# Performance work log

Measured on AMD Instinct MI355X. Metric: run time of the kernel, lower is better.

## Reference

```python
import jax, jax.numpy as jnp
import numpy as np

S, B, H2 = 2048, 16, 1024   # seq_len, batch, 2*hidden_dim
H = H2 // 2                  # hidden_dim
N = 4096                     # number of spans with nonempty tags
T = 8192                     # total number of target tags (ragged, flattened)
L = 256                      # label_dim
V = 50000                    # vocab size
GAMMA = 1.0


def setup_inputs() -> dict:
    key = jax.random.key(0)
    ks = jax.random.split(key, 10)
    hidden = jax.random.normal(ks[0], (S, B, H2), jnp.float32)
    W1 = jax.random.normal(ks[1], (L, H2), jnp.float32) * (1.0 / np.sqrt(H2))
    b1 = jnp.zeros((L,), jnp.float32)
    W2 = jax.random.normal(ks[2], (V, L), jnp.float32) * (1.0 / np.sqrt(L))
    b2 = jnp.zeros((V,), jnp.float32)
    span_bid = jax.random.randint(ks[3], (N,), 0, B, jnp.int32)
    span_begin = jax.random.randint(ks[4], (N,), 0, S, jnp.int32)
    span_end = jax.random.randint(ks[5], (N,), 0, S, jnp.int32)
    tag_span_id = jax.random.randint(ks[6], (T,), 0, N, jnp.int32)
    tags = jax.random.randint(ks[7], (T,), 0, V, jnp.int32)
    return {"hidden": hidden, "W1": W1, "b1": b1, "W2": W2, "b2": b2,
            "span_bid": span_bid, "span_begin": span_begin,
            "span_end": span_end, "tag_span_id": tag_span_id, "tags": tags}


def reference(hidden, W1, b1, W2, b2, span_bid, span_begin, span_end,
              tag_span_id, tags):
    # span embedding: forward half at begin-1 (wraps like torch negative idx),
    # backward half at end.  -> [N, 2H]
    fwd = hidden[(span_begin - 1) % S, span_bid, :H]
    bwd = hidden[span_end, span_bid, H:]
    feat = jnp.concatenate([fwd, bwd], axis=-1)          # [N, 2H]
    x = jnp.tanh(feat @ W1.T + b1)                       # [N, L]  (Linear+Tanh)
    logits = x @ W2.T + b2                               # [N, V]
    logp = jax.nn.log_softmax(logits, axis=-1)           # stable softmax->log
    pos_logp = logp[tag_span_id, tags]                   # [T] gathered targets
    pos = jnp.exp(pos_logp)                              # positive_probs
    # focal loss, gamma=1: -(1-p)^gamma * log(p), summed over all tags
    loss = jnp.sum(-((1.0 - pos) ** GAMMA) * pos_logp)
    loss = loss / (jnp.float32(T) + 1e-5)
    return loss.reshape(1)
```

## Files before the change

kernel.cpp:

```cpp
#include <hip/hip_runtime.h>
#include <hip/hip_fp8.h>

#define S_    2048
#define B_    16
#define H2_   1024
#define H_    512
#define N_    4096
#define T_    8192
#define L_    256
#define V_    50000
#define VPAD_ 50048

typedef float  floatx4 __attribute__((ext_vector_type(4)));
typedef __bf16 bf16x8  __attribute__((ext_vector_type(8)));

__device__ inline unsigned short f2bf(float f) {
  unsigned u = __builtin_bit_cast(unsigned, f);
  unsigned r = u + 0x7fffu + ((u >> 16) & 1u);
  return (unsigned short)(r >> 16);
}
__device__ inline float bf2f(unsigned short s) {
  unsigned u = ((unsigned)s) << 16;
  return __builtin_bit_cast(float, u);
}
__device__ inline unsigned char f2fp8(float f) {
  return (unsigned char)__hip_cvt_float_to_fp8(f, __HIP_SATFINITE, __HIP_E4M3);
}

__device__ inline void stage16(const void* g, void* l) {
  __builtin_amdgcn_global_load_lds(
      (const __attribute__((address_space(1))) void*)g,
      (__attribute__((address_space(3))) void*)l, 16, 0, 0);
}

__global__ __launch_bounds__(256) void gather_k(
    const float* __restrict__ hidden, const int* __restrict__ sbid,
    const int* __restrict__ sbeg, const int* __restrict__ send,
    unsigned short* __restrict__ featbf, float* __restrict__ lse) {
  const int n = blockIdx.x;
  const int t = threadIdx.x;
  if (t == 0) lse[n] = 0.f;
  if (n == 0 && t == 1) lse[N_] = 0.f;
  if (n == 0 && t == 2) ((unsigned*)lse)[N_ + 1] = 0u;
  const int bid = sbid[n];
  int r = sbeg[n] - 1; if (r < 0) r += S_;
  const int e = send[n];
  const size_t fbase = (size_t)r * (B_ * H2_) + (size_t)bid * H2_;
  const size_t bbase = (size_t)e * (B_ * H2_) + (size_t)bid * H2_;
  const int c = t * 4;
  const float4 v = (t < 128) ? *reinterpret_cast<const float4*>(hidden + fbase + c)
                             : *reinterpret_cast<const float4*>(hidden + bbase + c);
  unsigned short o[4];
  o[0] = f2bf(v.x); o[1] = f2bf(v.y); o[2] = f2bf(v.z); o[3] = f2bf(v.w);
  *reinterpret_cast<unsigned long long*>(featbf + (size_t)n * H2_ + c) =
      *reinterpret_cast<unsigned long long*>(o);
}

__global__ __launch_bounds__(256) void convert_k(
    const float* __restrict__ W1, const float* __restrict__ W2,
    const float* __restrict__ b2, unsigned short* __restrict__ w1b,
    unsigned char* __restrict__ w2f8, float* __restrict__ ebp) {
  const int gid = blockIdx.x * 256 + threadIdx.x;
  const int gstride = gridDim.x * 256;
  for (long j = (long)gid * 8; j < (long)VPAD_ * 256; j += (long)gstride * 8) {
    int row = (int)(j >> 8);
    unsigned char o[8];
    if (row < V_) {
#pragma unroll
      for (int q = 0; q < 8; q++) o[q] = f2fp8(W2[j + q]);
    } else {
#pragma unroll
      for (int q = 0; q < 8; q++) o[q] = 0;
    }
    *reinterpret_cast<unsigned long long*>(w2f8 + j) =
        *reinterpret_cast<unsigned long long*>(o);
  }
  for (int j = gid; j < L_ * H2_; j += gstride) w1b[j] = f2bf(W1[j]);
  for (int j = gid; j < VPAD_; j += gstride) ebp[j] = (j < V_) ? __expf(b2[j]) : 0.f;
}

__global__ __launch_bounds__(256) void gemm1_k(
    const unsigned short* __restrict__ A,
    const unsigned short* __restrict__ Bw,
    const float* __restrict__ b1,
    unsigned short* __restrict__ xbf,
    unsigned char* __restrict__ xf8) {
  __shared__ __align__(16) unsigned short sA[64 * 64];
  __shared__ __align__(16) unsigned short sB[64 * 64];
  const int tid   = threadIdx.x;
  const int mtile = (int)(blockIdx.x >> 2) * 64;
  const int ntile = (int)(blockIdx.x & 3) * 64;
  const int lane = tid & 63, wave = tid >> 6;
  const int wr = (wave & 1) * 32, wc = (wave >> 1) * 32;
  const int fr = lane & 15, fq = lane >> 4;
  floatx4 acc[2][2] = {};
  for (int k0 = 0; k0 < H2_; k0 += 64) {
#pragma unroll
    for (int i = 0; i < 2; i++) {
      const int slot = tid + i * 256;
      const int r = slot >> 3, cc = slot & 7;
      const int gk = cc ^ (r & 7);
      stage16(A  + (size_t)(mtile + r) * H2_ + k0 + gk * 8, &sA[slot * 8]);
      stage16(Bw + (size_t)(ntile + r) * H2_ + k0 + gk * 8, &sB[slot * 8]);
    }
    __syncthreads();
#pragma unroll
    for (int ks = 0; ks < 2; ks++) {
      bf16x8 av[2], bv[2];
#pragma unroll
      for (int mi = 0; mi < 2; mi++) {
        const int r = wr + mi * 16 + fr, kc = ks * 4 + fq;
        av[mi] = *reinterpret_cast<const bf16x8*>(&sA[(r * 8 + (kc ^ (r & 7))) * 8]);
      }
#pragma unroll
      for (int ni = 0; ni < 2; ni++) {
        const int r = wc + ni * 16 + fr, kc = ks * 4 + fq;
        bv[ni] = *reinterpret_cast<const bf16x8*>(&sB[(r * 8 + (kc ^ (r & 7))) * 8]);
      }
#pragma unroll
      for (int mi = 0; mi < 2; mi++)
#pragma unroll
        for (int ni = 0; ni < 2; ni++)
          acc[mi][ni] = __builtin_amdgcn_mfma_f32_16x16x32_bf16(av[mi], bv[ni], acc[mi][ni], 0, 0, 0);
    }
    __syncthreads();
  }
#pragma unroll
  for (int ni = 0; ni < 2; ni++) {
    const int col = ntile + wc + ni * 16 + fr;
    const float bias = b1[col];
#pragma unroll
    for (int mi = 0; mi < 2; mi++)
#pragma unroll
      for (int r = 0; r < 4; r++) {
        const int row = mtile + wr + mi * 16 + fq * 4 + r;
        const float t = tanhf(acc[mi][ni][r] + bias);
        xbf[(size_t)row * L_ + col] = f2bf(t);
        xf8[(size_t)row * L_ + col] = f2fp8(t);
      }
  }
}

__global__ __launch_bounds__(512, 2) void gemm2_k(
    const unsigned char* __restrict__ X8,
    const unsigned char* __restrict__ W8,
    const float* __restrict__ ebp,
    float* __restrict__ lse_sum) {
  __shared__ __align__(16) unsigned char sB[2][32768];
  const int tid   = threadIdx.x;
  const int mtile = ((int)blockIdx.x >> 4) * 128;
  const int strip = (int)blockIdx.x & 15;
  const int vt0   = (strip < 7) ? strip * 25 : 175 + (strip - 7) * 24;
  const int nt    = (strip < 7) ? 25 : 24;
  const int lane = tid & 63, wave = tid >> 6;
  const int wr = (wave & 1) * 64;
  const int wc = (wave >> 1) * 32;
  const int fr = lane & 15, fq = lane >> 4;

#pragma unroll
  for (int i = 0; i < 4; i++) {
    const int slot = tid + i * 512;
    const int r = slot >> 4, c = slot & 15;
    stage16(X8 + (size_t)(mtile + r) * 256 + ((c ^ (r & 15)) << 4), &sB[0][slot << 4]);
  }
  __syncthreads();
  long af[4][8];
#pragma unroll
  for (int mi = 0; mi < 4; mi++)
#pragma unroll
    for (int ks = 0; ks < 8; ks++) {
      const int r = wr + mi * 16 + fr;
      const int kb = ks * 32 + fq * 8;
      const int c = kb >> 4, o = kb & 15;
      af[mi][ks] = *reinterpret_cast<const long*>(
          &sB[0][(r << 8) + ((c ^ (r & 15)) << 4) + o]);
    }
  __syncthreads();

  float sacc[4][4];
#pragma unroll
  for (int mi = 0; mi < 4; mi++)
#pragma unroll
    for (int r = 0; r < 4; r++) sacc[mi][r] = 0.f;

  float eb_cur[2], eb_nxt[2];
#pragma unroll
  for (int ni = 0; ni < 2; ni++)
    eb_nxt[ni] = ebp[vt0 * 128 + wc + ni * 16 + fr];
  {
    const unsigned char* base = W8 + (size_t)vt0 * 128 * 256;
#pragma unroll
    for (int i = 0; i < 4; i++) {
      const int slot = tid + i * 512;
      const int r = slot >> 4, c = slot & 15;
      stage16(base + ((size_t)r << 8) + ((c ^ (r & 15)) << 4), &sB[0][slot << 4]);
    }
  }

  for (int j = 0; j < nt; j++) {
#pragma unroll
    for (int ni = 0; ni < 2; ni++) eb_cur[ni] = eb_nxt[ni];
    __syncthreads();
    if (j + 1 < nt) {
      const int vt = vt0 + j + 1;
#pragma unroll
      for (int ni = 0; ni < 2; ni++)
        eb_nxt[ni] = ebp[vt * 128 + wc + ni * 16 + fr];
      const unsigned char* base = W8 + (size_t)vt * 128 * 256;
      unsigned char* dst = &sB[(j + 1) & 1][0];
#pragma unroll
      for (int i = 0; i < 4; i++) {
        const int slot = tid + i * 512;
        const int r = slot >> 4, c = slot & 15;
        stage16(base + ((size_t)r << 8) + ((c ^ (r & 15)) << 4), dst + (slot << 4));
      }
    }

    const unsigned char* bb = &sB[j & 1][0];
    floatx4 acc[4][2] = {};
#pragma unroll
    for (int ks = 0; ks < 8; ks++) {
      long bv[2];
#pragma unroll
      for (int ni = 0; ni < 2; ni++) {
        const int r = wc + ni * 16 + fr;
        const int kb = ks * 32 + fq * 8;
        const int c = kb >> 4, o = kb & 15;
        bv[ni] = *reinterpret_cast<const long*>(
            &bb[(r << 8) + ((c ^ (r & 15)) << 4) + o]);
      }
#pragma unroll
      for (int mi = 0; mi < 4; mi++)
#pragma unroll
        for (int ni = 0; ni < 2; ni++)
          acc[mi][ni] = __builtin_amdgcn_mfma_f32_16x16x32_fp8_fp8(
              af[mi][ks], bv[ni], acc[mi][ni], 0, 0, 0);
    }
#pragma unroll
    for (int mi = 0; mi < 4; mi++)
#pragma unroll
      for (int r = 0; r < 4; r++) {
        float s = sacc[mi][r];
#pragma unroll
        for (int ni = 0; ni < 2; ni++)
          s = fmaf(eb_cur[ni], __expf(acc[mi][ni][r]), s);
        sacc[mi][r] = s;
      }
  }

#pragma unroll
  for (int mi = 0; mi < 4; mi++)
#pragma unroll
    for (int r = 0; r < 4; r++) {
      float s = sacc[mi][r];
      s += __shfl_xor(s, 1);
      s += __shfl_xor(s, 2);
      s += __shfl_xor(s, 4);
      s += __shfl_xor(s, 8);
      if (fr == 0)
        atomicAdd(&lse_sum[mtile + wr + mi * 16 + fq * 4 + r], s);
    }
}

__global__ __launch_bounds__(256) void loss_k(
    const unsigned short* __restrict__ xbf, const float* __restrict__ W2,
    const float* __restrict__ b2, const int* __restrict__ tsid,
    const int* __restrict__ tags, const float* __restrict__ lse_sum,
    float* __restrict__ loss_acc, unsigned* __restrict__ ticket,
    float* __restrict__ out) {
  const int lane = threadIdx.x & 63;
  const int gw = (int)(blockIdx.x * 256 + threadIdx.x) >> 6;
  const int nw = (int)(gridDim.x * 256) >> 6;
  float total = 0.f;
  for (int t = gw; t < T_; t += nw) {
    const int sid = tsid[t];
    const int v   = tags[t];
    const unsigned short* xr = xbf + (size_t)sid * L_;
    const float* w2r = W2 + (size_t)v * L_;
    float d = 0.f;
#pragma unroll
    for (int q = 0; q < 4; q++) {
      const int j = lane * 4 + q;
      d += bf2f(xr[j]) * w2r[j];
    }
#pragma unroll
    for (int m = 1; m < 64; m <<= 1) d += __shfl_xor(d, m);
    const float lp  = d + b2[v] - logf(lse_sum[sid]);
    const float pos = __expf(lp);
    total += (pos - 1.f) * lp;
  }
  if (lane == 0) atomicAdd(loss_acc, total);
  __syncthreads();
  __threadfence();
  if (threadIdx.x == 0) {
    const unsigned t = atomicAdd(ticket, 1u);
    if (t == (unsigned)gridDim.x - 1u) {
      const float v = atomicAdd(loss_acc, 0.0f);
      out[0] = v / (8192.0f + 1e-5f);
    }
  }
}

extern "C" void kernel_launch(void* const* d_in, const int* in_sizes, int n_in,
                              void* d_out, int out_size, void* d_ws, size_t ws_size,
                              hipStream_t stream) {
  const float* hidden = (const float*)d_in[0];
  const float* W1     = (const float*)d_in[1];
  const float* b1     = (const float*)d_in[2];
  const float* W2     = (const float*)d_in[3];
  const float* b2     = (const float*)d_in[4];
  const int* sbid = (const int*)d_in[5];
  const int* sbeg = (const int*)d_in[6];
  const int* send = (const int*)d_in[7];
  const int* tsid = (const int*)d_in[8];
  const int* tags = (const int*)d_in[9];
  float* out = (float*)d_out;

  char* ws = (char*)d_ws;
  unsigned short* featbf = (unsigned short*)(ws);
  unsigned short* xbf    = (unsigned short*)(ws + 8388608);
  unsigned short* w1bf   = (unsigned short*)(ws + 10485760);
  unsigned char*  xf8    = (unsigned char*) (ws + 11010048);
  unsigned char*  w2f8   = (unsigned char*) (ws + 12058624);
  float* ebp  = (float*)(ws + 24870912);
  float* lse  = (float*)(ws + 25071104);
  float* lacc = lse + N_;
  unsigned* ticket = (unsigned*)(lse + N_ + 1);

  gather_k<<<dim3(N_), dim3(256), 0, stream>>>(hidden, sbid, sbeg, send, featbf, lse);
  convert_k<<<dim3(4096), dim3(256), 0, stream>>>(W1, W2, b2, w1bf, w2f8, ebp);
  gemm1_k<<<dim3(256), dim3(256), 0, stream>>>(featbf, w1bf, b1, xbf, xf8);
  gemm2_k<<<dim3(512), dim3(512), 0, stream>>>(xf8, w2f8, ebp, lse);
  loss_k<<<dim3(256), dim3(256), 0, stream>>>(xbf, W2, b2, tsid, tags, lse, lacc, ticket, out);
}
```

Before: 352.8 us.

## Use scaled 16x16x128 FP8 MFMA in gemm2 with exp2 and reshaped wave tiling

```diff
diff --git a/kernel.cpp b/kernel.cpp
--- a/kernel.cpp
+++ b/kernel.cpp
@@ -11,8 +11,12 @@
 #define V_    50000
 #define VPAD_ 50048
 
+#define LOG2E_ 1.44269504088896f
+
 typedef float  floatx4 __attribute__((ext_vector_type(4)));
 typedef __bf16 bf16x8  __attribute__((ext_vector_type(8)));
+typedef int    intx4   __attribute__((ext_vector_type(4)));
+typedef int    intx8   __attribute__((ext_vector_type(8)));
 
 __device__ inline unsigned short f2bf(float f) {
   unsigned u = __builtin_bit_cast(unsigned, f);
@@ -67,7 +71,7 @@
     unsigned char o[8];
     if (row < V_) {
 #pragma unroll
-      for (int q = 0; q < 8; q++) o[q] = f2fp8(W2[j + q]);
+      for (int q = 0; q < 8; q++) o[q] = f2fp8(W2[j + q] * LOG2E_);
     } else {
 #pragma unroll
       for (int q = 0; q < 8; q++) o[q] = 0;
@@ -141,7 +145,7 @@
   }
 }
 
-__global__ __launch_bounds__(512, 2) void gemm2_k(
+__global__ __launch_bounds__(512, 4) void gemm2_k(
     const unsigned char* __restrict__ X8,
     const unsigned char* __restrict__ W8,
     const float* __restrict__ ebp,
@@ -153,8 +157,8 @@
   const int vt0   = (strip < 7) ? strip * 25 : 175 + (strip - 7) * 24;
   const int nt    = (strip < 7) ? 25 : 24;
   const int lane = tid & 63, wave = tid >> 6;
-  const int wr = (wave & 1) * 64;
-  const int wc = (wave >> 1) * 32;
+  const int wr = (wave & 3) * 32;
+  const int wc = (wave >> 2) * 64;
   const int fr = lane & 15, fq = lane >> 4;
 
 #pragma unroll
@@ -164,28 +168,29 @@
     stage16(X8 + (size_t)(mtile + r) * 256 + ((c ^ (r & 15)) << 4), &sB[0][slot << 4]);
   }
   __syncthreads();
-  long af[4][8];
-#pragma unroll
-  for (int mi = 0; mi < 4; mi++)
-#pragma unroll
-    for (int ks = 0; ks < 8; ks++) {
-      const int r = wr + mi * 16 + fr;
-      const int kb = ks * 32 + fq * 8;
-      const int c = kb >> 4, o = kb & 15;
-      af[mi][ks] = *reinterpret_cast<const long*>(
-          &sB[0][(r << 8) + ((c ^ (r & 15)) << 4) + o]);
+  intx8 af[2][2];
+#pragma unroll
+  for (int mi = 0; mi < 2; mi++)
+#pragma unroll
+    for (int kh = 0; kh < 2; kh++) {
+      const int r  = wr + mi * 16 + fr;
+      const int c0 = kh * 8 + fq * 2;
+      *reinterpret_cast<intx4*>(&af[mi][kh]) =
+          *reinterpret_cast<const intx4*>(&sB[0][(r << 8) + ((c0 ^ (r & 15)) << 4)]);
+      *(reinterpret_cast<intx4*>(&af[mi][kh]) + 1) =
+          *reinterpret_cast<const intx4*>(&sB[0][(r << 8) + (((c0 + 1) ^ (r & 15)) << 4)]);
     }
   __syncthreads();
 
-  float sacc[4][4];
-#pragma unroll
-  for (int mi = 0; mi < 4; mi++)
+  float sacc[2][4];
+#pragma unroll
+  for (int mi = 0; mi < 2; mi++)
 #pragma unroll
     for (int r = 0; r < 4; r++) sacc[mi][r] = 0.f;
 
-  float eb_cur[2], eb_nxt[2];
-#pragma unroll
-  for (int ni = 0; ni < 2; ni++)
+  float eb_cur[4], eb_nxt[4];
+#pragma unroll
+  for (int ni = 0; ni < 4; ni++)
     eb_nxt[ni] = ebp[vt0 * 128 + wc + ni * 16 + fr];
   {
     const unsigned char* base = W8 + (size_t)vt0 * 128 * 256;
@@ -199,12 +204,12 @@
 
   for (int j = 0; j < nt; j++) {
 #pragma unroll
-    for (int ni = 0; ni < 2; ni++) eb_cur[ni] = eb_nxt[ni];
+    for (int ni = 0; ni < 4; ni++) eb_cur[ni] = eb_nxt[ni];
     __syncthreads();
     if (j + 1 < nt) {
       const int vt = vt0 + j + 1;
 #pragma unroll
-      for (int ni = 0; ni < 2; ni++)
+      for (int ni = 0; ni < 4; ni++)
         eb_nxt[ni] = ebp[vt * 128 + wc + ni * 16 + fr];
       const unsigned char* base = W8 + (size_t)vt * 128 * 256;
       unsigned char* dst = &sB[(j + 1) & 1][0];
@@ -217,39 +222,39 @@
     }
 
     const unsigned char* bb = &sB[j & 1][0];
-    floatx4 acc[4][2] = {};
-#pragma unroll
-    for (int ks = 0; ks < 8; ks++) {
-      long bv[2];
-#pragma unroll
-      for (int ni = 0; ni < 2; ni++) {
-        const int r = wc + ni * 16 + fr;
-        const int kb = ks * 32 + fq * 8;
-        const int c = kb >> 4, o = kb & 15;
-        bv[ni] = *reinterpret_cast<const long*>(
-            &bb[(r << 8) + ((c ^ (r & 15)) << 4) + o]);
-      }
-#pragma unroll
-      for (int mi = 0; mi < 4; mi++)
-#pragma unroll
-        for (int ni = 0; ni < 2; ni++)
-          acc[mi][ni] = __builtin_amdgcn_mfma_f32_16x16x32_fp8_fp8(
-              af[mi][ks], bv[ni], acc[mi][ni], 0, 0, 0);
-    }
-#pragma unroll
-    for (int mi = 0; mi < 4; mi++)
+    floatx4 acc[2][4] = {};
+#pragma unroll
+    for (int kh = 0; kh < 2; kh++) {
+#pragma unroll
+      for (int ni = 0; ni < 4; ni++) {
+        intx8 bv;
+        const int r  = wc + ni * 16 + fr;
+        const int c0 = kh * 8 + fq * 2;
+        *reinterpret_cast<intx4*>(&bv) =
+            *reinterpret_cast<const intx4*>(&bb[(r << 8) + ((c0 ^ (r & 15)) << 4)]);
+        *(reinterpret_cast<intx4*>(&bv) + 1) =
+            *reinterpret_cast<const intx4*>(&bb[(r << 8) + (((c0 + 1) ^ (r & 15)) << 4)]);
+#pragma unroll
+        for (int mi = 0; mi < 2; mi++)
+          acc[mi][ni] = __builtin_amdgcn_mfma_scale_f32_16x16x128_f8f6f4(
+              af[mi][kh], bv, acc[mi][ni], 0, 0,
+              0, 0x7f7f7f7f, 0, 0x7f7f7f7f);
+      }
+    }
+#pragma unroll
+    for (int mi = 0; mi < 2; mi++)
 #pragma unroll
       for (int r = 0; r < 4; r++) {
         float s = sacc[mi][r];
 #pragma unroll
-        for (int ni = 0; ni < 2; ni++)
-          s = fmaf(eb_cur[ni], __expf(acc[mi][ni][r]), s);
+        for (int ni = 0; ni < 4; ni++)
+          s = fmaf(eb_cur[ni], __builtin_amdgcn_exp2f(acc[mi][ni][r]), s);
         sacc[mi][r] = s;
       }
   }
 
 #pragma unroll
-  for (int mi = 0; mi < 4; mi++)
+  for (int mi = 0; mi < 2; mi++)
 #pragma unroll
     for (int r = 0; r < 4; r++) {
       float s = sacc[mi][r];
```

Result: faster. 310.4 us (-12.0%).
